# Performance work log

Measured on AMD Instinct MI355X. Metric: run time of the kernel, lower is better.

Reference implementation:

```python
import jax, jax.numpy as jnp
import numpy as np

C_IN = 256
C_INTER = C_IN // 2  # max(1, C//2)
B, D, H, W = 2, 16, 64, 64


def setup_inputs() -> dict:
    key = jax.random.key(0)
    ks = jax.random.split(key, 9)
    s = 1.0 / np.sqrt(C_IN)
    si = 1.0 / np.sqrt(C_INTER)
    return {
        "x": jax.random.normal(ks[0], (B, C_IN, D, H, W), dtype=jnp.float32),
        # 1x1x1 conv weights reduce to [out, in] matrices
        "g_w": jax.random.normal(ks[1], (C_INTER, C_IN), dtype=jnp.float32) * s,
        "g_b": jax.random.normal(ks[2], (C_INTER,), dtype=jnp.float32) * s,
        "theta_w": jax.random.normal(ks[3], (C_INTER, C_IN), dtype=jnp.float32) * s,
        "theta_b": jax.random.normal(ks[4], (C_INTER,), dtype=jnp.float32) * s,
        "phi_w": jax.random.normal(ks[5], (C_INTER, C_IN), dtype=jnp.float32) * s,
        "phi_b": jax.random.normal(ks[6], (C_INTER,), dtype=jnp.float32) * s,
        # note: torch code inits W to zero; random here so gradients/outputs are non-trivial
        "W_w": jax.random.normal(ks[7], (C_IN, C_INTER), dtype=jnp.float32) * si,
        "W_b": jax.random.normal(ks[8], (C_IN,), dtype=jnp.float32) * si,
    }


def reference(x, g_w, g_b, theta_w, theta_b, phi_w, phi_b, W_w, W_b):
    b, c, d, h, w = x.shape
    n = d * h * w
    xf = x.reshape(b, c, n)  # [B, C, N]
    # 1x1x1 convs == per-position linear projections
    g = jnp.einsum('oc,bcn->bon', g_w, xf) + g_b[None, :, None]        # [B, Ci, N]
    th = jnp.einsum('oc,bcn->bon', theta_w, xf) + theta_b[None, :, None]
    ph = jnp.einsum('oc,bcn->bon', phi_w, xf) + phi_b[None, :, None]
    # f = theta^T @ phi (N x N), y = (f / N) @ g^T. Since the normalizer is a
    # constant, reassociate: kv = phi @ g^T is [Ci, Ci], avoiding the NxN matrix.
    kv = jnp.einsum('bin,bjn->bij', ph, g)                              # [B, Ci, Ci]
    y = jnp.einsum('bin,bij->bjn', th, kv) / n                          # [B, Ci, N]
    y = jnp.einsum('oc,bcn->bon', W_w, y) + W_b[None, :, None]          # [B, C, N]
    return x + y.reshape(b, c, d, h, w)
```

## Files before the change

kernel.cpp:

```cpp
#include <hip/hip_runtime.h>

#define NB 2
#define CC 256
#define CI 128
#define NN 65536
#define LDA 72
#define LDX 264

typedef __bf16 bf16x8 __attribute__((ext_vector_type(8)));
typedef float f32x4 __attribute__((ext_vector_type(4)));

__device__ __forceinline__ unsigned short f2bf(float f) {
  unsigned u = __float_as_uint(f);
  u += 0x7fffu + ((u >> 16) & 1u);
  return (unsigned short)(u >> 16);
}

__global__ __launch_bounds__(512) void nl3d_syrk2(const float* __restrict__ x,
                                                  float* __restrict__ S,
                                                  float* __restrict__ partials,
                                                  float* __restrict__ svec,
                                                  int kchunk, int use_partial) {
  __shared__ unsigned short lds[2][256 * LDA];
  const int tid = threadIdx.x;
  const int lane = tid & 63;
  const int wv = tid >> 6;
  const int wm = wv & 3, wn = wv >> 2;
  const int b = blockIdx.y;
  const int kc0 = blockIdx.x * kchunk;

  const float* xb = x + (size_t)b * CC * NN;
  f32x4 acc[4][8];
  const f32x4 zero4 = {0.f, 0.f, 0.f, 0.f};
#pragma unroll
  for (int i = 0; i < 4; ++i)
#pragma unroll
    for (int j = 0; j < 8; ++j) acc[i][j] = zero4;

  float rsum[8];
#pragma unroll
  for (int i = 0; i < 8; ++i) rsum[i] = 0.f;

  const int r0 = tid >> 4;
  const int c4 = tid & 15;
  const int m = lane & 15;
  const int kg = (lane >> 4) * 8;

  const int stages = kchunk >> 6;

  {
    float4 f[8];
#pragma unroll
    for (int i = 0; i < 8; ++i)
      f[i] = *(const float4*)(xb + (size_t)(r0 + 32 * i) * NN + kc0 + c4 * 4);
#pragma unroll
    for (int i = 0; i < 8; ++i) {
      int row = r0 + 32 * i;
      ushort4 h;
      h.x = f2bf(f[i].x); h.y = f2bf(f[i].y); h.z = f2bf(f[i].z); h.w = f2bf(f[i].w);
      *(ushort4*)&lds[0][row * LDA + c4 * 4] = h;
      rsum[i] += f[i].x + f[i].y + f[i].z + f[i].w;
    }
  }
  __syncthreads();

  int cur = 0;
  for (int s = 0; s < stages; ++s) {
    float4 g[8];
    const bool pf = (s + 1 < stages);
    if (pf) {
      const int kc = kc0 + (s + 1) * 64;
#pragma unroll
      for (int i = 0; i < 8; ++i)
        g[i] = *(const float4*)(xb + (size_t)(r0 + 32 * i) * NN + kc + c4 * 4);
    }

    const unsigned short* L = lds[cur];
#pragma unroll
    for (int kk = 0; kk < 2; ++kk) {
      bf16x8 afr[4], bfr[8];
#pragma unroll
      for (int mt = 0; mt < 4; ++mt)
        afr[mt] = *(const bf16x8*)&L[(wm * 64 + mt * 16 + m) * LDA + kk * 32 + kg];
#pragma unroll
      for (int nt = 0; nt < 8; ++nt)
        bfr[nt] = *(const bf16x8*)&L[(wn * 128 + nt * 16 + m) * LDA + kk * 32 + kg];
#pragma unroll
      for (int mt = 0; mt < 4; ++mt)
#pragma unroll
        for (int nt = 0; nt < 8; ++nt)
          acc[mt][nt] = __builtin_amdgcn_mfma_f32_16x16x32_bf16(bfr[nt], afr[mt], acc[mt][nt], 0, 0, 0);
    }

    if (pf) {
      unsigned short* Lw = (unsigned short*)lds[cur ^ 1];
#pragma unroll
      for (int i = 0; i < 8; ++i) {
        int row = r0 + 32 * i;
        ushort4 h;
        h.x = f2bf(g[i].x); h.y = f2bf(g[i].y); h.z = f2bf(g[i].z); h.w = f2bf(g[i].w);
        *(ushort4*)&Lw[row * LDA + c4 * 4] = h;
        rsum[i] += g[i].x + g[i].y + g[i].z + g[i].w;
      }
    }
    __syncthreads();
    cur ^= 1;
  }

  const int col = lane & 15;
  const int rq = (lane >> 4) * 4;
  if (use_partial) {
    float* dst = partials + ((size_t)(b * gridDim.x + blockIdx.x)) * (CC * CC);
#pragma unroll
    for (int mt = 0; mt < 4; ++mt) {
      const int gi = wm * 64 + mt * 16 + col;
#pragma unroll
      for (int nt = 0; nt < 8; ++nt) {
        const int gj = wn * 128 + nt * 16 + rq;
        float4 v;
        v.x = acc[mt][nt][0]; v.y = acc[mt][nt][1];
        v.z = acc[mt][nt][2]; v.w = acc[mt][nt][3];
        *(float4*)&dst[(size_t)gi * CC + gj] = v;
      }
    }
  } else {
    float* Sb = S + (size_t)b * CC * CC;
#pragma unroll
    for (int mt = 0; mt < 4; ++mt)
#pragma unroll
      for (int nt = 0; nt < 8; ++nt)
#pragma unroll
        for (int r = 0; r < 4; ++r) {
          int gi = wm * 64 + mt * 16 + col;
          int gj = wn * 128 + nt * 16 + rq + r;
          atomicAdd(&Sb[(size_t)gi * CC + gj], acc[mt][nt][r]);
        }
  }

  __syncthreads();
  float* ldsRS = (float*)lds[0];
  if (tid < 256) ldsRS[tid] = 0.f;
  __syncthreads();
#pragma unroll
  for (int i = 0; i < 8; ++i) atomicAdd(&ldsRS[r0 + 32 * i], rsum[i]);
  __syncthreads();
  if (tid < 256) atomicAdd(&svec[b * CC + tid], ldsRS[tid]);
}

__global__ __launch_bounds__(128) void nl3d_reduce(const float* __restrict__ partials,
                                                   float* __restrict__ S, int splits) {
  const int e = blockIdx.x * 128 + threadIdx.x;
  const int b = e >> 14;
  const int off = e & 16383;
  const float4* p = (const float4*)partials;
  float4 a0 = {0, 0, 0, 0}, a1 = {0, 0, 0, 0}, a2 = {0, 0, 0, 0}, a3 = {0, 0, 0, 0};
  const size_t base = (size_t)b * splits * 16384 + off;
  for (int s = 0; s < splits; s += 4) {
    float4 v0 = p[base + (size_t)s * 16384];
    float4 v1 = p[base + (size_t)(s + 1) * 16384];
    float4 v2 = p[base + (size_t)(s + 2) * 16384];
    float4 v3 = p[base + (size_t)(s + 3) * 16384];
    a0.x += v0.x; a0.y += v0.y; a0.z += v0.z; a0.w += v0.w;
    a1.x += v1.x; a1.y += v1.y; a1.z += v1.z; a1.w += v1.w;
    a2.x += v2.x; a2.y += v2.y; a2.z += v2.z; a2.w += v2.w;
    a3.x += v3.x; a3.y += v3.y; a3.z += v3.z; a3.w += v3.w;
  }
  float4 r;
  r.x = (a0.x + a1.x) + (a2.x + a3.x);
  r.y = (a0.y + a1.y) + (a2.y + a3.y);
  r.z = (a0.z + a1.z) + (a2.z + a3.z);
  r.w = (a0.w + a1.w) + (a2.w + a3.w);
  ((float4*)S)[e] = r;
}

__global__ void nl3d_b1(const float* __restrict__ phi_w, const float* __restrict__ S,
                        const float* __restrict__ g_w, float* __restrict__ gwT,
                        float* __restrict__ P) {
  if (threadIdx.x < 128) {
    int t = blockIdx.x * 128 + threadIdx.x;
    int j = t >> 8, d2 = t & 255;
    gwT[d2 * CI + j] = g_w[t];
  }
  int b = blockIdx.x >> 7, i = blockIdx.x & 127, d = threadIdx.x;
  const float* Sb = S + (size_t)b * CC * CC;
  const float* ph = phi_w + i * CC;
  float a0 = 0.f, a1 = 0.f, a2 = 0.f, a3 = 0.f;
  float a4 = 0.f, a5 = 0.f, a6 = 0.f, a7 = 0.f;
  for (int c = 0; c < CC; c += 8) {
    a0 += ph[c + 0] * Sb[(c + 0) * CC + d];
    a1 += ph[c + 1] * Sb[(c + 1) * CC + d];
    a2 += ph[c + 2] * Sb[(c + 2) * CC + d];
    a3 += ph[c + 3] * Sb[(c + 3) * CC + d];
    a4 += ph[c + 4] * Sb[(c + 4) * CC + d];
    a5 += ph[c + 5] * Sb[(c + 5) * CC + d];
    a6 += ph[c + 6] * Sb[(c + 6) * CC + d];
    a7 += ph[c + 7] * Sb[(c + 7) * CC + d];
  }
  P[((size_t)b * CI + i) * CC + d] =
      ((a0 + a1) + (a2 + a3)) + ((a4 + a5) + (a6 + a7));
}

__global__ void nl3d_b2(const float* __restrict__ P, const float* __restrict__ gwT,
                        const float* __restrict__ svec, const float* __restrict__ phi_w,
                        const float* __restrict__ phi_b, const float* __restrict__ g_b,
                        float* __restrict__ kv) {
  int b = blockIdx.x >> 7, i = blockIdx.x & 127, j = threadIdx.x;
  const float* Pr = P + ((size_t)b * CI + i) * CC;
  const float* sv = svec + b * CC;
  const float* ph = phi_w + i * CC;
  float u0 = 0.f, u1 = 0.f, u2 = 0.f, u3 = 0.f;
  for (int c = 0; c < CC; c += 4) {
    u0 += ph[c] * sv[c];
    u1 += ph[c + 1] * sv[c + 1];
    u2 += ph[c + 2] * sv[c + 2];
    u3 += ph[c + 3] * sv[c + 3];
  }
  float a0 = 0.f, a1 = 0.f, a2 = 0.f, a3 = 0.f;
  float v0 = 0.f, v1 = 0.f, v2 = 0.f, v3 = 0.f;
  for (int d = 0; d < CC; d += 4) {
    float gT0 = gwT[d * CI + j],       gT1 = gwT[(d + 1) * CI + j];
    float gT2 = gwT[(d + 2) * CI + j], gT3 = gwT[(d + 3) * CI + j];
    a0 += Pr[d] * gT0;     a1 += Pr[d + 1] * gT1;
    a2 += Pr[d + 2] * gT2; a3 += Pr[d + 3] * gT3;
    v0 += sv[d] * gT0;     v1 += sv[d + 1] * gT1;
    v2 += sv[d + 2] * gT2; v3 += sv[d + 3] * gT3;
  }
  kv[((size_t)b * CI + i) * CI + j] =
      ((a0 + a1) + (a2 + a3)) + ((u0 + u1) + (u2 + u3)) * g_b[j] +
      phi_b[i] * (((v0 + v1) + (v2 + v3)) + (float)NN * g_b[j]);
}

__global__ void nl3d_b3(const float* __restrict__ kv, const float* __restrict__ theta_w,
                        const float* __restrict__ theta_b, float* __restrict__ T2,
                        float* __restrict__ tb2) {
  int b = blockIdx.x >> 7, j = blockIdx.x & 127, c = threadIdx.x;
  const float* kvb = kv + (size_t)b * CI * CI;
  float a0 = 0.f, a1 = 0.f, a2 = 0.f, a3 = 0.f;
  for (int i = 0; i < CI; i += 4) {
    a0 += kvb[i * CI + j] * theta_w[i * CC + c];
    a1 += kvb[(i + 1) * CI + j] * theta_w[(i + 1) * CC + c];
    a2 += kvb[(i + 2) * CI + j] * theta_w[(i + 2) * CC + c];
    a3 += kvb[(i + 3) * CI + j] * theta_w[(i + 3) * CC + c];
  }
  T2[((size_t)b * CI + j) * CC + c] = (a0 + a1) + (a2 + a3);
  if (c == 0) {
    float t = 0.f;
    for (int i = 0; i < CI; ++i) t += kvb[i * CI + j] * theta_b[i];
    tb2[b * CI + j] = t;
  }
}

__global__ void nl3d_b4(const float* __restrict__ T2, const float* __restrict__ tb2,
                        const float* __restrict__ W_w, const float* __restrict__ W_b,
                        unsigned short* __restrict__ Mbf, float* __restrict__ cvec) {
  int b = blockIdx.x >> 8, o = blockIdx.x & 255, c = threadIdx.x;
  const float inv = 1.0f / (float)NN;
  const float* Wr = W_w + o * CI;
  float a0 = 0.f, a1 = 0.f, a2 = 0.f, a3 = 0.f;
  for (int j = 0; j < CI; j += 4) {
    a0 += Wr[j] * T2[((size_t)b * CI + j) * CC + c];
    a1 += Wr[j + 1] * T2[((size_t)b * CI + j + 1) * CC + c];
    a2 += Wr[j + 2] * T2[((size_t)b * CI + j + 2) * CC + c];
    a3 += Wr[j + 3] * T2[((size_t)b * CI + j + 3) * CC + c];
  }
  Mbf[((size_t)b * CC + o) * CC + c] = f2bf(((a0 + a1) + (a2 + a3)) * inv);
  if (c == 0) {
    float t = 0.f;
    for (int j = 0; j < CI; ++j) t += Wr[j] * tb2[b * CI + j];
    cvec[b * CC + o] = t * inv + W_b[o];
  }
}

__global__ __launch_bounds__(256) void nl3d_out(const float* __restrict__ x,
                                                const unsigned short* __restrict__ Mbf,
                                                const float* __restrict__ cvec,
                                                float* __restrict__ out) {
  __shared__ unsigned short xT[64 * LDX];
  const int tid = threadIdx.x;
  const int lane = tid & 63;
  const int wv = tid >> 6;
  const int b = blockIdx.y;
  const int n0 = blockIdx.x * 64;

  const float* xb = x + (size_t)b * CC * NN;
  float* ob = out + (size_t)b * CC * NN;

  {
    const int c4 = tid & 15;
    const int t4 = tid >> 4;
    float4 f0[8], f1[8];
#pragma unroll
    for (int i = 0; i < 8; ++i) {
      int p = i * 16 + t4;
      f0[i] = *(const float4*)(xb + (size_t)(2 * p) * NN + n0 + c4 * 4);
      f1[i] = *(const float4*)(xb + (size_t)(2 * p + 1) * NN + n0 + c4 * 4);
    }
#pragma unroll
    for (int i = 0; i < 8; ++i) {
      int p = i * 16 + t4;
      int ps = p ^ ((c4 & 7) << 2);
      float a0[4] = {f0[i].x, f0[i].y, f0[i].z, f0[i].w};
      float a1[4] = {f1[i].x, f1[i].y, f1[i].z, f1[i].w};
#pragma unroll
      for (int j = 0; j < 4; ++j) {
        unsigned pack = (unsigned)f2bf(a0[j]) | ((unsigned)f2bf(a1[j]) << 16);
        *(unsigned*)&xT[(c4 * 4 + j) * LDX + 2 * ps] = pack;
      }
    }
  }
  __syncthreads();

  f32x4 acc[4][4];
  const f32x4 zero4 = {0.f, 0.f, 0.f, 0.f};
#pragma unroll
  for (int i = 0; i < 4; ++i)
#pragma unroll
    for (int j = 0; j < 4; ++j) acc[i][j] = zero4;

  const int m = lane & 15;
  const int kg = (lane >> 4) * 8;
  const unsigned short* Mb = Mbf + (size_t)b * CC * CC;

  bf16x8 afr[4];
#pragma unroll
  for (int mt = 0; mt < 4; ++mt)
    afr[mt] = *(const bf16x8*)(Mb + (size_t)(wv * 64 + mt * 16 + m) * CC + kg);
#pragma unroll
  for (int kc = 0; kc < 8; ++kc) {
    bf16x8 cur[4];
#pragma unroll
    for (int mt = 0; mt < 4; ++mt) cur[mt] = afr[mt];
    if (kc < 7) {
#pragma unroll
      for (int mt = 0; mt < 4; ++mt)
        afr[mt] = *(const bf16x8*)(Mb + (size_t)(wv * 64 + mt * 16 + m) * CC + (kc + 1) * 32 + kg);
    }
    bf16x8 bfr[4];
#pragma unroll
    for (int nt = 0; nt < 4; ++nt) {
      int rr = nt * 16 + m;
      int d0 = (kc * 16 + (kg >> 1)) ^ (((rr >> 2) & 7) << 2);
      bfr[nt] = *(const bf16x8*)&xT[rr * LDX + 2 * d0];
    }
#pragma unroll
    for (int mt = 0; mt < 4; ++mt)
#pragma unroll
      for (int nt = 0; nt < 4; ++nt)
        acc[mt][nt] = __builtin_amdgcn_mfma_f32_16x16x32_bf16(cur[mt], bfr[nt], acc[mt][nt], 0, 0, 0);
  }

  const int col = lane & 15;
  const int rquad = (lane >> 4) * 4;
#pragma unroll
  for (int mt = 0; mt < 4; ++mt)
#pragma unroll
    for (int r = 0; r < 4; ++r) {
      int o = wv * 64 + mt * 16 + rquad + r;
      float cv = cvec[b * CC + o];
      const float* xrow = xb + (size_t)o * NN + n0;
      float* orow = ob + (size_t)o * NN + n0;
#pragma unroll
      for (int nt = 0; nt < 4; ++nt) {
        int n = nt * 16 + col;
        orow[n] = xrow[n] + acc[mt][nt][r] + cv;
      }
    }
}

extern "C" void kernel_launch(void* const* d_in, const int* in_sizes, int n_in,
                              void* d_out, int out_size, void* d_ws, size_t ws_size,
                              hipStream_t stream) {
  const float* x       = (const float*)d_in[0];
  const float* g_w     = (const float*)d_in[1];
  const float* g_b     = (const float*)d_in[2];
  const float* theta_w = (const float*)d_in[3];
  const float* theta_b = (const float*)d_in[4];
  const float* phi_w   = (const float*)d_in[5];
  const float* phi_b   = (const float*)d_in[6];
  const float* W_w     = (const float*)d_in[7];
  const float* W_b     = (const float*)d_in[8];
  float* out = (float*)d_out;

  char* ws = (char*)d_ws;
  float* S    = (float*)(ws);
  float* svec = (float*)(ws + 524288);
  float* P    = (float*)(ws + 526336);
  float* gwT  = (float*)(ws + 788480);
  float* kv   = (float*)(ws + 919552);
  float* T2   = (float*)(ws + 1050624);
  float* tb2  = (float*)(ws + 1312768);
  unsigned short* Mbf = (unsigned short*)(ws + 1313792);
  float* cvec = (float*)(ws + 1575936);
  float* partials = (float*)(ws + 2097152);

  int splits = 0;
  for (int c = 128; c >= 8; c >>= 1) {
    if (2097152 + (size_t)NB * c * CC * CC * 4 <= ws_size) { splits = c; break; }
  }

  if (splits > 0) {
    hipMemsetAsync(svec, 0, 2048, stream);
    nl3d_syrk2<<<dim3(splits, NB), 512, 0, stream>>>(x, S, partials, svec,
                                                     NN / splits, 1);
    nl3d_reduce<<<256, 128, 0, stream>>>(partials, S, splits);
  } else {
    hipMemsetAsync(ws, 0, 526336, stream);
    nl3d_syrk2<<<dim3(64, NB), 512, 0, stream>>>(x, S, (float*)ws, svec,
                                                 NN / 64, 0);
  }
  nl3d_b1<<<NB * CI, 256, 0, stream>>>(phi_w, S, g_w, gwT, P);
  nl3d_b2<<<NB * CI, 128, 0, stream>>>(P, gwT, svec, phi_w, phi_b, g_b, kv);
  nl3d_b3<<<NB * CI, 256, 0, stream>>>(kv, theta_w, theta_b, T2, tb2);
  nl3d_b4<<<NB * CC, 256, 0, stream>>>(T2, tb2, W_w, W_b, Mbf, cvec);
  nl3d_out<<<dim3(NN / 64, NB), 256, 0, stream>>>(x, Mbf, cvec, out);
}
```

Before: 392.0 us.

## Fuse small kv kernels and split output GEMM across 8 waves

Merges the two small kernels that compute kv into one, keeping the intermediate P row and svec in shared memory and reading g_w rows directly instead of a transposed copy. This removes one launch and the P and gwT global round trips. The output kernel moves from 256 to 512 threads, splitting each 64-column tile across two wave groups so each wave computes 4x2 MFMA tiles instead of 4x4. The A-fragment software prefetch is dropped. The aim is more waves in flight to hide memory latency in the bandwidth-bound output pass, at the cost of reloading the M fragments in both wave groups.

```diff
diff --git a/kernel.cpp b/kernel.cpp
--- a/kernel.cpp
+++ b/kernel.cpp
@@ -173,15 +173,17 @@
   ((float4*)S)[e] = r;
 }
 
-__global__ void nl3d_b1(const float* __restrict__ phi_w, const float* __restrict__ S,
-                        const float* __restrict__ g_w, float* __restrict__ gwT,
-                        float* __restrict__ P) {
-  if (threadIdx.x < 128) {
-    int t = blockIdx.x * 128 + threadIdx.x;
-    int j = t >> 8, d2 = t & 255;
-    gwT[d2 * CI + j] = g_w[t];
-  }
-  int b = blockIdx.x >> 7, i = blockIdx.x & 127, d = threadIdx.x;
+__global__ __launch_bounds__(256) void nl3d_b12(const float* __restrict__ phi_w,
+                                                const float* __restrict__ S,
+                                                const float* __restrict__ svec,
+                                                const float* __restrict__ g_w,
+                                                const float* __restrict__ phi_b,
+                                                const float* __restrict__ g_b,
+                                                float* __restrict__ kv) {
+  __shared__ float Prow[CC];
+  __shared__ float svl[CC];
+  const int b = blockIdx.x >> 7, i = blockIdx.x & 127;
+  const int d = threadIdx.x;
   const float* Sb = S + (size_t)b * CC * CC;
   const float* ph = phi_w + i * CC;
   float a0 = 0.f, a1 = 0.f, a2 = 0.f, a3 = 0.f;
@@ -196,38 +198,31 @@
     a6 += ph[c + 6] * Sb[(c + 6) * CC + d];
     a7 += ph[c + 7] * Sb[(c + 7) * CC + d];
   }
-  P[((size_t)b * CI + i) * CC + d] =
-      ((a0 + a1) + (a2 + a3)) + ((a4 + a5) + (a6 + a7));
-}
-
-__global__ void nl3d_b2(const float* __restrict__ P, const float* __restrict__ gwT,
-                        const float* __restrict__ svec, const float* __restrict__ phi_w,
-                        const float* __restrict__ phi_b, const float* __restrict__ g_b,
-                        float* __restrict__ kv) {
-  int b = blockIdx.x >> 7, i = blockIdx.x & 127, j = threadIdx.x;
-  const float* Pr = P + ((size_t)b * CI + i) * CC;
-  const float* sv = svec + b * CC;
-  const float* ph = phi_w + i * CC;
-  float u0 = 0.f, u1 = 0.f, u2 = 0.f, u3 = 0.f;
-  for (int c = 0; c < CC; c += 4) {
-    u0 += ph[c] * sv[c];
-    u1 += ph[c + 1] * sv[c + 1];
-    u2 += ph[c + 2] * sv[c + 2];
-    u3 += ph[c + 3] * sv[c + 3];
-  }
-  float a0 = 0.f, a1 = 0.f, a2 = 0.f, a3 = 0.f;
-  float v0 = 0.f, v1 = 0.f, v2 = 0.f, v3 = 0.f;
-  for (int d = 0; d < CC; d += 4) {
-    float gT0 = gwT[d * CI + j],       gT1 = gwT[(d + 1) * CI + j];
-    float gT2 = gwT[(d + 2) * CI + j], gT3 = gwT[(d + 3) * CI + j];
-    a0 += Pr[d] * gT0;     a1 += Pr[d + 1] * gT1;
-    a2 += Pr[d + 2] * gT2; a3 += Pr[d + 3] * gT3;
-    v0 += sv[d] * gT0;     v1 += sv[d + 1] * gT1;
-    v2 += sv[d + 2] * gT2; v3 += sv[d + 3] * gT3;
-  }
-  kv[((size_t)b * CI + i) * CI + j] =
-      ((a0 + a1) + (a2 + a3)) + ((u0 + u1) + (u2 + u3)) * g_b[j] +
-      phi_b[i] * (((v0 + v1) + (v2 + v3)) + (float)NN * g_b[j]);
+  Prow[d] = ((a0 + a1) + (a2 + a3)) + ((a4 + a5) + (a6 + a7));
+  svl[d] = svec[b * CC + d];
+  __syncthreads();
+
+  if (d < CI) {
+    const int j = d;
+    const float* gr = g_w + (size_t)j * CC;
+    float p0 = 0.f, p1 = 0.f, p2 = 0.f, p3 = 0.f;
+    float v0 = 0.f, v1 = 0.f, v2 = 0.f, v3 = 0.f;
+    float u0 = 0.f, u1 = 0.f, u2 = 0.f, u3 = 0.f;
+    for (int c = 0; c < CC; c += 4) {
+      float g0 = gr[c], g1 = gr[c + 1], g2 = gr[c + 2], g3 = gr[c + 3];
+      p0 += Prow[c] * g0;     p1 += Prow[c + 1] * g1;
+      p2 += Prow[c + 2] * g2; p3 += Prow[c + 3] * g3;
+      v0 += svl[c] * g0;      v1 += svl[c + 1] * g1;
+      v2 += svl[c + 2] * g2;  v3 += svl[c + 3] * g3;
+      u0 += ph[c] * svl[c];       u1 += ph[c + 1] * svl[c + 1];
+      u2 += ph[c + 2] * svl[c + 2]; u3 += ph[c + 3] * svl[c + 3];
+    }
+    float a = (p0 + p1) + (p2 + p3);
+    float v = (v0 + v1) + (v2 + v3);
+    float u = (u0 + u1) + (u2 + u3);
+    kv[((size_t)b * CI + i) * CI + j] =
+        a + u * g_b[j] + phi_b[i] * (v + (float)NN * g_b[j]);
+  }
 }
 
 __global__ void nl3d_b3(const float* __restrict__ kv, const float* __restrict__ theta_w,
@@ -271,7 +266,7 @@
   }
 }
 
-__global__ __launch_bounds__(256) void nl3d_out(const float* __restrict__ x,
+__global__ __launch_bounds__(512) void nl3d_out(const float* __restrict__ x,
                                                 const unsigned short* __restrict__ Mbf,
                                                 const float* __restrict__ cvec,
                                                 float* __restrict__ out) {
@@ -279,6 +274,8 @@
   const int tid = threadIdx.x;
   const int lane = tid & 63;
   const int wv = tid >> 6;
+  const int wm = wv & 3;
+  const int wn = wv >> 2;
   const int b = blockIdx.y;
   const int n0 = blockIdx.x * 64;
 
@@ -288,16 +285,16 @@
   {
     const int c4 = tid & 15;
     const int t4 = tid >> 4;
-    float4 f0[8], f1[8];
-#pragma unroll
-    for (int i = 0; i < 8; ++i) {
-      int p = i * 16 + t4;
+    float4 f0[4], f1[4];
+#pragma unroll
+    for (int i = 0; i < 4; ++i) {
+      int p = i * 32 + t4;
       f0[i] = *(const float4*)(xb + (size_t)(2 * p) * NN + n0 + c4 * 4);
       f1[i] = *(const float4*)(xb + (size_t)(2 * p + 1) * NN + n0 + c4 * 4);
     }
 #pragma unroll
-    for (int i = 0; i < 8; ++i) {
-      int p = i * 16 + t4;
+    for (int i = 0; i < 4; ++i) {
+      int p = i * 32 + t4;
       int ps = p ^ ((c4 & 7) << 2);
       float a0[4] = {f0[i].x, f0[i].y, f0[i].z, f0[i].w};
       float a1[4] = {f1[i].x, f1[i].y, f1[i].z, f1[i].w};
@@ -310,43 +307,33 @@
   }
   __syncthreads();
 
-  f32x4 acc[4][4];
+  f32x4 acc[4][2];
   const f32x4 zero4 = {0.f, 0.f, 0.f, 0.f};
 #pragma unroll
   for (int i = 0; i < 4; ++i)
 #pragma unroll
-    for (int j = 0; j < 4; ++j) acc[i][j] = zero4;
+    for (int j = 0; j < 2; ++j) acc[i][j] = zero4;
 
   const int m = lane & 15;
   const int kg = (lane >> 4) * 8;
   const unsigned short* Mb = Mbf + (size_t)b * CC * CC;
-
-  bf16x8 afr[4];
-#pragma unroll
-  for (int mt = 0; mt < 4; ++mt)
-    afr[mt] = *(const bf16x8*)(Mb + (size_t)(wv * 64 + mt * 16 + m) * CC + kg);
 #pragma unroll
   for (int kc = 0; kc < 8; ++kc) {
-    bf16x8 cur[4];
-#pragma unroll
-    for (int mt = 0; mt < 4; ++mt) cur[mt] = afr[mt];
-    if (kc < 7) {
-#pragma unroll
-      for (int mt = 0; mt < 4; ++mt)
-        afr[mt] = *(const bf16x8*)(Mb + (size_t)(wv * 64 + mt * 16 + m) * CC + (kc + 1) * 32 + kg);
-    }
-    bf16x8 bfr[4];
-#pragma unroll
-    for (int nt = 0; nt < 4; ++nt) {
-      int rr = nt * 16 + m;
+    bf16x8 afr[4], bfr[2];
+#pragma unroll
+    for (int mt = 0; mt < 4; ++mt)
+      afr[mt] = *(const bf16x8*)(Mb + (size_t)(wm * 64 + mt * 16 + m) * CC + kc * 32 + kg);
+#pragma unroll
+    for (int nt = 0; nt < 2; ++nt) {
+      int rr = wn * 32 + nt * 16 + m;
       int d0 = (kc * 16 + (kg >> 1)) ^ (((rr >> 2) & 7) << 2);
       bfr[nt] = *(const bf16x8*)&xT[rr * LDX + 2 * d0];
     }
 #pragma unroll
     for (int mt = 0; mt < 4; ++mt)
 #pragma unroll
-      for (int nt = 0; nt < 4; ++nt)
-        acc[mt][nt] = __builtin_amdgcn_mfma_f32_16x16x32_bf16(cur[mt], bfr[nt], acc[mt][nt], 0, 0, 0);
+      for (int nt = 0; nt < 2; ++nt)
+        acc[mt][nt] = __builtin_amdgcn_mfma_f32_16x16x32_bf16(afr[mt], bfr[nt], acc[mt][nt], 0, 0, 0);
   }
 
   const int col = lane & 15;
@@ -355,13 +342,13 @@
   for (int mt = 0; mt < 4; ++mt)
 #pragma unroll
     for (int r = 0; r < 4; ++r) {
-      int o = wv * 64 + mt * 16 + rquad + r;
+      int o = wm * 64 + mt * 16 + rquad + r;
       float cv = cvec[b * CC + o];
       const float* xrow = xb + (size_t)o * NN + n0;
       float* orow = ob + (size_t)o * NN + n0;
 #pragma unroll
-      for (int nt = 0; nt < 4; ++nt) {
-        int n = nt * 16 + col;
+      for (int nt = 0; nt < 2; ++nt) {
+        int n = wn * 32 + nt * 16 + col;
         orow[n] = xrow[n] + acc[mt][nt][r] + cv;
       }
     }
@@ -384,8 +371,6 @@
   char* ws = (char*)d_ws;
   float* S    = (float*)(ws);
   float* svec = (float*)(ws + 524288);
-  float* P    = (float*)(ws + 526336);
-  float* gwT  = (float*)(ws + 788480);
   float* kv   = (float*)(ws + 919552);
   float* T2   = (float*)(ws + 1050624);
   float* tb2  = (float*)(ws + 1312768);
@@ -408,9 +393,8 @@
     nl3d_syrk2<<<dim3(64, NB), 512, 0, stream>>>(x, S, (float*)ws, svec,
                                                  NN / 64, 0);
   }
-  nl3d_b1<<<NB * CI, 256, 0, stream>>>(phi_w, S, g_w, gwT, P);
-  nl3d_b2<<<NB * CI, 128, 0, stream>>>(P, gwT, svec, phi_w, phi_b, g_b, kv);
+  nl3d_b12<<<NB * CI, 256, 0, stream>>>(phi_w, S, svec, g_w, phi_b, g_b, kv);
   nl3d_b3<<<NB * CI, 256, 0, stream>>>(kv, theta_w, theta_b, T2, tb2);
   nl3d_b4<<<NB * CC, 256, 0, stream>>>(T2, tb2, W_w, W_b, Mbf, cvec);
-  nl3d_out<<<dim3(NN / 64, NB), 256, 0, stream>>>(x, Mbf, cvec, out);
-}
+  nl3d_out<<<dim3(NN / 64, NB), 512, 0, stream>>>(x, Mbf, cvec, out);
+}
```

Result: slower. 409.4 us (+4.4%).
